# Performance work log

Measured on AMD Instinct MI355X. Metric: run time of the kernel, lower is better.

## Reference

```python
import jax, jax.numpy as jnp
import numpy as np


def setup_inputs() -> dict:
    key = jax.random.key(0)
    ks = jax.random.split(key, 6)
    dim, dt_rank, dim_inner, d_state, channels, batch = 1024, 64, 1024, 128, 64, 8
    rn = lambda k, shape, sc: (jax.random.normal(k, shape, jnp.float32) * sc)
    return {
        "x": rn(ks[0], (batch, channels, dim), 1.0),
        "proj_w": rn(ks[1], (dim, dim), dim ** -0.5),
        "proj_b": jnp.zeros((dim,), jnp.float32),
        "conv_w": rn(ks[2], (channels, channels, 3), (channels * 3) ** -0.5),
        "conv_b": jnp.zeros((channels,), jnp.float32),
        "deltaBC_w": rn(ks[3], (dt_rank + 2 * d_state, dim), dim ** -0.5),
        "dt_proj_w": rn(ks[4], (dim_inner, dt_rank), dt_rank ** -0.5),
        "dt_proj_b": jnp.zeros((dim_inner,), jnp.float32),
        "A_log": jnp.log(jnp.broadcast_to(
            jnp.arange(1, d_state + 1, dtype=jnp.float32), (dim_inner, d_state))),
        "D": jnp.ones((dim_inner,), jnp.float32),
    }


def _silu(x):
    return x * jax.nn.sigmoid(x)


def _selective_scan(x, delta, A, B, C, D):
    # x, delta: (b, l, ed); A: (ed, n); B, C: (b, l, n); D: (ed)
    deltaA = jnp.exp(delta[..., None] * A)                      # (b, l, ed, n)
    BX = delta[..., None] * B[:, :, None, :] * x[..., None]     # (b, l, ed, n)

    def binop(e1, e2):
        a1, b1 = e1
        a2, b2 = e2
        return a1 * a2, a2 * b1 + b2

    # h_t = deltaA_t * h_{t-1} + BX_t  (parallel scan over sequence axis)
    _, hs = jax.lax.associative_scan(binop, (deltaA, BX), axis=1)
    y = jnp.einsum("blen,bln->ble", hs, C) + D * x
    return y


def reference(x, proj_w, proj_b, conv_w, conv_b, deltaBC_w,
              dt_proj_w, dt_proj_b, A_log, D):
    dt_rank = dt_proj_w.shape[1]
    d_state = A_log.shape[1]

    skip = x
    # same self.proj applied to both branches
    x1 = x @ proj_w.T + proj_b
    x2 = x1

    # Conv1d over the feature axis, treating seq positions as channels (L == channels)
    x1 = jax.lax.conv_general_dilated(
        x1, conv_w, window_strides=(1,), padding=[(1, 1)],
        dimension_numbers=("NCH", "OIH", "NCH")) + conv_b[None, :, None]
    x1 = _silu(x1)

    # SSM
    A = -jnp.exp(A_log)
    dbc = x1 @ deltaBC_w.T                                      # (b, l, dt_rank + 2n)
    delta = dbc[..., :dt_rank]
    Bm = dbc[..., dt_rank:dt_rank + d_state]
    Cm = dbc[..., dt_rank + d_state:]
    delta = jax.nn.softplus(delta @ dt_proj_w.T + dt_proj_b)    # (b, l, ed)
    y = _selective_scan(x1, delta, A, Bm, Cm, D)

    out = y * _silu(x2) + skip
    return out @ proj_w.T + proj_b
```

## Files before the change

### kernel.cpp

```cpp
#include <hip/hip_runtime.h>
#include <hip/hip_bf16.h>
#include <math.h>

typedef __hip_bfloat16 bf16;
typedef __attribute__((ext_vector_type(8))) short bf16x8;
typedef __attribute__((ext_vector_type(4))) float f32x4;

#define DIM     1024
#define DT_RANK 64
#define D_STATE 128
#define CHAN    64
#define BATCH   8
#define ROWS    (BATCH*CHAN)
#define DBC_N   (DT_RANK + 2*D_STATE)

#define SZ_X    (ROWS*DIM)
#define SZ_PW   (DIM*DIM)
#define SZ_PB   (DIM)
#define SZ_CW   (CHAN*CHAN*3)
#define SZ_CB   (CHAN)
#define SZ_DBCW (DBC_N*DIM)
#define SZ_DTW  (DIM*DT_RANK)
#define SZ_DTB  (DIM)
#define SZ_ALOG (DIM*D_STATE)
#define SZ_D    (DIM)

#define O0 0
#define O1 (O0+SZ_X)
#define O2 (O1+SZ_PW)
#define O3 (O2+SZ_PB)
#define O4 (O3+SZ_CW)
#define O5 (O4+SZ_CB)
#define O6 (O5+SZ_DBCW)
#define O7 (O6+SZ_DTW)
#define O8 (O7+SZ_DTB)
#define O9 (O8+SZ_ALOG)
#define TOTAL (O9+SZ_D)

__device__ __forceinline__ unsigned short f2b(float v) {
    bf16 t = __float2bfloat16(v);
    return *reinterpret_cast<unsigned short*>(&t);
}
__device__ __forceinline__ float b162f(unsigned short s) {
    return __uint_as_float(((unsigned)s) << 16);
}

__global__ __launch_bounds__(256) void convert_kernel(
    const void* __restrict__ s0, const void* __restrict__ s1,
    const void* __restrict__ s2, const void* __restrict__ s3,
    const void* __restrict__ s4, const void* __restrict__ s5,
    const void* __restrict__ s6, const void* __restrict__ s7,
    const void* __restrict__ s8, const void* __restrict__ s9,
    float* __restrict__ dstf, bf16* __restrict__ dstb,
    int* __restrict__ flag, const unsigned* __restrict__ dsrc)
{
    const int isb = (dsrc[0] == 0x3F803F80u) ? 1 : 0;
    if (blockIdx.x == 0 && threadIdx.x == 0) *flag = isb;
    int idx = (blockIdx.x * 256 + threadIdx.x) * 4;
    if (idx >= TOTAL) return;
    const void* src; int base;
    if      (idx < O1) { src = s0; base = O0; }
    else if (idx < O2) { src = s1; base = O1; }
    else if (idx < O3) { src = s2; base = O2; }
    else if (idx < O4) { src = s3; base = O3; }
    else if (idx < O5) { src = s4; base = O4; }
    else if (idx < O6) { src = s5; base = O5; }
    else if (idx < O7) { src = s6; base = O6; }
    else if (idx < O8) { src = s7; base = O7; }
    else if (idx < O9) { src = s8; base = O8; }
    else               { src = s9; base = O9; }
    const int rel = idx - base;
    float4 v;
    if (isb) {
        ushort4 s = *reinterpret_cast<const ushort4*>((const bf16*)src + rel);
        v.x = b162f(s.x); v.y = b162f(s.y); v.z = b162f(s.z); v.w = b162f(s.w);
    } else {
        v = *reinterpret_cast<const float4*>((const float*)src + rel);
    }
    *reinterpret_cast<float4*>(&dstf[idx]) = v;
    ushort4 u; u.x = f2b(v.x); u.y = f2b(v.y); u.z = f2b(v.z); u.w = f2b(v.w);
    *reinterpret_cast<ushort4*>(&dstb[idx]) = u;
}

template<int ACT, int OUTMODE, int K>
__global__ __launch_bounds__(256) void gemm_mfma(
    const bf16* __restrict__ A, const bf16* __restrict__ B,
    const float* __restrict__ bias, void* __restrict__ C0, bf16* __restrict__ C1,
    int lda, int ldb, int ldc, const int* __restrict__ flagp)
{
    __shared__ float red[4][32][36];
    const int l  = threadIdx.x & 63;
    const int w  = threadIdx.x >> 6;
    const int m0 = blockIdx.y * 32;
    const int n0 = blockIdx.x * 32;
    const int fr = l & 15;
    const int ko = (l >> 4) * 8;

    const bf16* Abase = A + (size_t)(m0 + fr) * lda + ko;
    const bf16* Bbase = B + (size_t)(n0 + fr) * ldb + ko;

    f32x4 acc00 = {}, acc01 = {}, acc10 = {}, acc11 = {};

    #pragma unroll 4
    for (int ks = w; ks * 32 < K; ks += 4) {
        const int k0 = ks * 32;
        bf16x8 a0 = *reinterpret_cast<const bf16x8*>(Abase + k0);
        bf16x8 a1 = *reinterpret_cast<const bf16x8*>(Abase + (size_t)16 * lda + k0);
        bf16x8 b0 = *reinterpret_cast<const bf16x8*>(Bbase + k0);
        bf16x8 b1 = *reinterpret_cast<const bf16x8*>(Bbase + (size_t)16 * ldb + k0);
        acc00 = __builtin_amdgcn_mfma_f32_16x16x32_bf16(a0, b0, acc00, 0, 0, 0);
        acc01 = __builtin_amdgcn_mfma_f32_16x16x32_bf16(a0, b1, acc01, 0, 0, 0);
        acc10 = __builtin_amdgcn_mfma_f32_16x16x32_bf16(a1, b0, acc10, 0, 0, 0);
        acc11 = __builtin_amdgcn_mfma_f32_16x16x32_bf16(a1, b1, acc11, 0, 0, 0);
    }

    {
        const int cr = (l >> 4) * 4;
        const int cc = l & 15;
        #pragma unroll
        for (int v = 0; v < 4; ++v) {
            red[w][cr + v][cc]           = acc00[v];
            red[w][cr + v][16 + cc]      = acc01[v];
            red[w][16 + cr + v][cc]      = acc10[v];
            red[w][16 + cr + v][16 + cc] = acc11[v];
        }
    }
    __syncthreads();

    const int t = threadIdx.x;
    const int r = t >> 3;
    const int c = (t & 7) * 4;
    float o[4];
    #pragma unroll
    for (int q = 0; q < 4; ++q) {
        float s = red[0][r][c + q] + red[1][r][c + q]
                + red[2][r][c + q] + red[3][r][c + q];
        if (bias) s += bias[n0 + c + q];
        if (ACT == 1) s = (s > 20.0f) ? s : log1pf(__expf(s));
        o[q] = s;
    }
    const int m = m0 + r, nn = n0 + c;
    const size_t off = (size_t)m * ldc + nn;
    if (OUTMODE == 0) {
        *reinterpret_cast<float4*>((float*)C0 + off) = make_float4(o[0], o[1], o[2], o[3]);
    } else if (OUTMODE == 2) {
        *reinterpret_cast<float4*>((float*)C0 + off) = make_float4(o[0], o[1], o[2], o[3]);
        ushort4 u; u.x = f2b(o[0]); u.y = f2b(o[1]); u.z = f2b(o[2]); u.w = f2b(o[3]);
        *reinterpret_cast<ushort4*>(C1 + off) = u;
    } else {
        if (*flagp) {
            ushort4 u; u.x = f2b(o[0]); u.y = f2b(o[1]); u.z = f2b(o[2]); u.w = f2b(o[3]);
            *reinterpret_cast<ushort4*>((bf16*)C0 + off) = u;
        } else {
            *reinterpret_cast<float4*>((float*)C0 + off) = make_float4(o[0], o[1], o[2], o[3]);
        }
    }
}

__global__ __launch_bounds__(256) void conv_silu_kernel(
    const float* __restrict__ xin, const float* __restrict__ cw,
    const float* __restrict__ cb, float* __restrict__ xout,
    bf16* __restrict__ xout_bf)
{
    const int o   = blockIdx.x;
    const int n   = blockIdx.y;
    const int tid = threadIdx.x;
    const int h0  = tid * 4;
    const float* xrow = xin + (size_t)n * CHAN * DIM;
    const float* wrow = cw + o * CHAN * 3;
    float acc0 = 0.f, acc1 = 0.f, acc2 = 0.f, acc3 = 0.f;
    #pragma unroll 4
    for (int i = 0; i < CHAN; ++i) {
        const float* xr = xrow + (size_t)i * DIM;
        const float4 xv = *reinterpret_cast<const float4*>(&xr[h0]);
        const float left  = (h0 > 0)        ? xr[h0 - 1] : 0.0f;
        const float right = (h0 + 4 < DIM)  ? xr[h0 + 4] : 0.0f;
        const float w0 = wrow[i * 3 + 0];
        const float w1 = wrow[i * 3 + 1];
        const float w2 = wrow[i * 3 + 2];
        acc0 = fmaf(left, w0, fmaf(xv.x, w1, fmaf(xv.y, w2, acc0)));
        acc1 = fmaf(xv.x, w0, fmaf(xv.y, w1, fmaf(xv.z, w2, acc1)));
        acc2 = fmaf(xv.y, w0, fmaf(xv.z, w1, fmaf(xv.w, w2, acc2)));
        acc3 = fmaf(xv.z, w0, fmaf(xv.w, w1, fmaf(right, w2, acc3)));
    }
    const float bb = cb[o];
    size_t base = (size_t)(n * CHAN + o) * DIM + h0;
    float v0 = acc0 + bb, v1 = acc1 + bb, v2 = acc2 + bb, v3 = acc3 + bb;
    v0 = v0 / (1.0f + __expf(-v0));
    v1 = v1 / (1.0f + __expf(-v1));
    v2 = v2 / (1.0f + __expf(-v2));
    v3 = v3 / (1.0f + __expf(-v3));
    *reinterpret_cast<float4*>(&xout[base]) = make_float4(v0, v1, v2, v3);
    ushort4 u; u.x = f2b(v0); u.y = f2b(v1); u.z = f2b(v2); u.w = f2b(v3);
    *reinterpret_cast<ushort4*>(&xout_bf[base]) = u;
}

__device__ __forceinline__ float sum8_dpp(float x) {
    int v;
    v = __builtin_amdgcn_update_dpp(0, __float_as_int(x), 0x111, 0xf, 0xf, true);
    x += __int_as_float(v);
    v = __builtin_amdgcn_update_dpp(0, __float_as_int(x), 0x112, 0xf, 0xf, true);
    x += __int_as_float(v);
    v = __builtin_amdgcn_update_dpp(0, __float_as_int(x), 0x114, 0xf, 0xf, true);
    x += __int_as_float(v);
    return x;
}

#define EPW 2
__global__ __launch_bounds__(256) void scan_kernel(
    const float* __restrict__ xskip,
    const float* __restrict__ x2,
    const float* __restrict__ xc,
    const float* __restrict__ dbc,
    const float* __restrict__ delta,
    const float* __restrict__ A_log,
    const float* __restrict__ Dp,
    bf16*        __restrict__ outp)
{
    __shared__ float sDB[4][CHAN][4];
    __shared__ float sPart[4][EPW][CHAN][8];
    const int w    = threadIdx.x >> 6;
    const int lane = threadIdx.x & 63;
    const int bb   = blockIdx.x >> 7;
    const int eb   = (blockIdx.x & 127) * (4 * EPW) + w * EPW;
    const int r0   = bb * CHAN;
    const int r    = r0 + lane;

    const float2 dlt2 = *reinterpret_cast<const float2*>(&delta[(size_t)r * DIM + eb]);
    const float2 xv2  = *reinterpret_cast<const float2*>(&xc   [(size_t)r * DIM + eb]);
    const float2 x22  = *reinterpret_cast<const float2*>(&x2   [(size_t)r * DIM + eb]);
    const float2 xs2  = *reinterpret_cast<const float2*>(&xskip[(size_t)r * DIM + eb]);
    const float2 dv2  = *reinterpret_cast<const float2*>(&Dp[eb]);

    const float C_LOG2E = 1.44269504f;
    const float2 alA = *reinterpret_cast<const float2*>(&A_log[(size_t)(eb    ) * D_STATE + 2 * lane]);
    const float2 alB = *reinterpret_cast<const float2*>(&A_log[(size_t)(eb + 1) * D_STATE + 2 * lane]);
    const float a00 = -__expf(alA.x) * C_LOG2E;
    const float a01 = -__expf(alA.y) * C_LOG2E;
    const float a10 = -__expf(alB.x) * C_LOG2E;
    const float a11 = -__expf(alB.y) * C_LOG2E;
    const float ga0 = x22.x / (1.0f + __expf(-x22.x));
    const float ga1 = x22.y / (1.0f + __expf(-x22.y));
    const float fb0 = fmaf(dv2.x * xv2.x, ga0, xs2.x);
    const float fb1 = fmaf(dv2.y * xv2.y, ga1, xs2.y);

    *reinterpret_cast<float4*>(&sDB[w][lane][0]) =
        make_float4(dlt2.x, dlt2.x * xv2.x, dlt2.y, dlt2.y * xv2.y);
    __syncthreads();

    float h00 = 0.f, h01 = 0.f, h10 = 0.f, h11 = 0.f;
    const float* bp = dbc + (size_t)r0 * DBC_N + DT_RANK + 2 * lane;
    const float* cp = bp + D_STATE;
    float2 bv = *reinterpret_cast<const float2*>(bp);
    float2 cv = *reinterpret_cast<const float2*>(cp);

    #pragma unroll 4
    for (int l = 0; l < CHAN; ++l) {
        const float* bpn = bp + ((l < CHAN - 1) ? DBC_N : 0);
        const float* cpn = cp + ((l < CHAN - 1) ? DBC_N : 0);
        const float2 bn = *reinterpret_cast<const float2*>(bpn);
        const float2 cn = *reinterpret_cast<const float2*>(cpn);

        const float4 d = *reinterpret_cast<const float4*>(&sDB[w][l][0]);

        const float e00 = exp2f(d.x * a00);
        const float e01 = exp2f(d.x * a01);
        h00 = fmaf(e00, h00, d.y * bv.x);
        h01 = fmaf(e01, h01, d.y * bv.y);
        const float p0 = sum8_dpp(fmaf(h00, cv.x, h01 * cv.y));

        const float e10 = exp2f(d.z * a10);
        const float e11 = exp2f(d.z * a11);
        h10 = fmaf(e10, h10, d.w * bv.x);
        h11 = fmaf(e11, h11, d.w * bv.y);
        const float p1 = sum8_dpp(fmaf(h10, cv.x, h11 * cv.y));

        if ((lane & 7) == 7) {
            const int q = lane >> 3;
            sPart[w][0][l][q] = p0;
            sPart[w][1][l][q] = p1;
        }
        bp = bpn; cp = cpn; bv = bn; cv = cn;
    }
    __syncthreads();

    const float4 q0 = *reinterpret_cast<const float4*>(&sPart[w][0][lane][0]);
    const float4 q1 = *reinterpret_cast<const float4*>(&sPart[w][0][lane][4]);
    const float4 q2 = *reinterpret_cast<const float4*>(&sPart[w][1][lane][0]);
    const float4 q3 = *reinterpret_cast<const float4*>(&sPart[w][1][lane][4]);
    const float y0 = ((q0.x + q0.y) + (q0.z + q0.w)) + ((q1.x + q1.y) + (q1.z + q1.w));
    const float y1 = ((q2.x + q2.y) + (q2.z + q2.w)) + ((q3.x + q3.y) + (q3.z + q3.w));
    ushort2 u;
    u.x = f2b(fmaf(y0, ga0, fb0));
    u.y = f2b(fmaf(y1, ga1, fb1));
    *reinterpret_cast<ushort2*>(&outp[(size_t)r * DIM + eb]) = u;
}

extern "C" void kernel_launch(void* const* d_in, const int* in_sizes, int n_in,
                              void* d_out, int out_size, void* d_ws, size_t ws_size,
                              hipStream_t stream) {
    float* ws   = (float*)d_ws;
    int*   flag = (int*)d_ws;
    float* inF  = ws + 16;
    bf16*  inB  = (bf16*)(inF + TOTAL);

    float* x1_pre = (float*)(inB + TOTAL);
    float* x1c    = x1_pre + (size_t)ROWS * DIM;
    bf16*  x1c_bf = (bf16*)(x1c + (size_t)ROWS * DIM);
    float* dbc    = (float*)(x1c_bf + (size_t)ROWS * DIM);
    bf16*  dbc_bf = (bf16*)(dbc + (size_t)ROWS * DBC_N);
    float* delta  = (float*)(dbc_bf + (size_t)ROWS * DBC_N);
    bf16*  outp_bf= (bf16*)(delta + (size_t)ROWS * DIM);

    convert_kernel<<<(TOTAL / 4 + 255) / 256, 256, 0, stream>>>(
        d_in[0], d_in[1], d_in[2], d_in[3], d_in[4],
        d_in[5], d_in[6], d_in[7], d_in[8], d_in[9],
        inF, inB, flag, (const unsigned*)d_in[9]);

    gemm_mfma<0, 0, DIM><<<dim3(DIM / 32, ROWS / 32), 256, 0, stream>>>(
        inB + O0, inB + O1, inF + O2, x1_pre, nullptr, DIM, DIM, DIM, nullptr);
    conv_silu_kernel<<<dim3(CHAN, BATCH), 256, 0, stream>>>(x1_pre, inF + O3, inF + O4, x1c, x1c_bf);
    gemm_mfma<0, 2, DIM><<<dim3(DBC_N / 32, ROWS / 32), 256, 0, stream>>>(
        x1c_bf, inB + O5, nullptr, dbc, dbc_bf, DIM, DIM, DBC_N, nullptr);
    gemm_mfma<1, 0, DT_RANK><<<dim3(DIM / 32, ROWS / 32), 256, 0, stream>>>(
        dbc_bf, inB + O6, inF + O7, delta, nullptr, DBC_N, DT_RANK, DIM, nullptr);
    scan_kernel<<<dim3(BATCH * (DIM / (4 * EPW))), 256, 0, stream>>>(
        inF + O0, x1_pre, x1c, dbc, delta, inF + O8, inF + O9, outp_bf);
    gemm_mfma<0, 1, DIM><<<dim3(DIM / 32, ROWS / 32), 256, 0, stream>>>(
        outp_bf, inB + O1, inF + O2, d_out, nullptr, DIM, DIM, DIM, flag);
}
```

Before: 96.52 us.

## Stage bf16 B/C in LDS for scan, drop fp32 dbc and x copies

The scan kernel now loads the B/C columns of dbc as bf16 into shared memory once per block and reads them from LDS. Each lane now owns states lane and lane+64 instead of a contiguous pair, so the per-step reduction becomes a full 64-lane DPP sum with a single lane writing y, replacing the 8-way partials. The fp32 dbc output of the deltaBC GEMM, the fp32 copies of x and proj_w from the convert kernel, and the fp32 skip read are all dropped. This cuts global traffic and writes, but B/C and the skip term are now consumed at bf16 precision, and the longer DPP chain adds latency on each scan step.

```diff
diff --git a/kernel.cpp b/kernel.cpp
--- a/kernel.cpp
+++ b/kernel.cpp
@@ -77,7 +77,8 @@
     } else {
         v = *reinterpret_cast<const float4*>((const float*)src + rel);
     }
-    *reinterpret_cast<float4*>(&dstf[idx]) = v;
+    if (idx >= O2)
+        *reinterpret_cast<float4*>(&dstf[idx]) = v;
     ushort4 u; u.x = f2b(v.x); u.y = f2b(v.y); u.z = f2b(v.z); u.w = f2b(v.w);
     *reinterpret_cast<ushort4*>(&dstb[idx]) = u;
 }
@@ -145,6 +146,9 @@
         *reinterpret_cast<float4*>((float*)C0 + off) = make_float4(o[0], o[1], o[2], o[3]);
     } else if (OUTMODE == 2) {
         *reinterpret_cast<float4*>((float*)C0 + off) = make_float4(o[0], o[1], o[2], o[3]);
+        ushort4 u; u.x = f2b(o[0]); u.y = f2b(o[1]); u.z = f2b(o[2]); u.w = f2b(o[3]);
+        *reinterpret_cast<ushort4*>(C1 + off) = u;
+    } else if (OUTMODE == 3) {
         ushort4 u; u.x = f2b(o[0]); u.y = f2b(o[1]); u.z = f2b(o[2]); u.w = f2b(o[3]);
         *reinterpret_cast<ushort4*>(C1 + off) = u;
     } else {
@@ -195,104 +199,106 @@
     *reinterpret_cast<ushort4*>(&xout_bf[base]) = u;
 }
 
-__device__ __forceinline__ float sum8_dpp(float x) {
+__device__ __forceinline__ float sum64_dpp(float x) {
     int v;
-    v = __builtin_amdgcn_update_dpp(0, __float_as_int(x), 0x111, 0xf, 0xf, true);
-    x += __int_as_float(v);
-    v = __builtin_amdgcn_update_dpp(0, __float_as_int(x), 0x112, 0xf, 0xf, true);
-    x += __int_as_float(v);
-    v = __builtin_amdgcn_update_dpp(0, __float_as_int(x), 0x114, 0xf, 0xf, true);
-    x += __int_as_float(v);
+    v = __builtin_amdgcn_update_dpp(0, __float_as_int(x), 0x111, 0xf, 0xf, true); x += __int_as_float(v);
+    v = __builtin_amdgcn_update_dpp(0, __float_as_int(x), 0x112, 0xf, 0xf, true); x += __int_as_float(v);
+    v = __builtin_amdgcn_update_dpp(0, __float_as_int(x), 0x114, 0xf, 0xf, true); x += __int_as_float(v);
+    v = __builtin_amdgcn_update_dpp(0, __float_as_int(x), 0x118, 0xf, 0xf, true); x += __int_as_float(v);
+    v = __builtin_amdgcn_update_dpp(0, __float_as_int(x), 0x142, 0xa, 0xf, true); x += __int_as_float(v);
+    v = __builtin_amdgcn_update_dpp(0, __float_as_int(x), 0x143, 0xc, 0xf, true); x += __int_as_float(v);
     return x;
 }
 
 #define EPW 2
+#define SBPAD 264
 __global__ __launch_bounds__(256) void scan_kernel(
-    const float* __restrict__ xskip,
+    const bf16*  __restrict__ xskip_bf,
     const float* __restrict__ x2,
     const float* __restrict__ xc,
-    const float* __restrict__ dbc,
+    const bf16*  __restrict__ dbc_bf,
     const float* __restrict__ delta,
     const float* __restrict__ A_log,
     const float* __restrict__ Dp,
     bf16*        __restrict__ outp)
 {
+    __shared__ unsigned short sBC[CHAN][SBPAD];
     __shared__ float sDB[4][CHAN][4];
-    __shared__ float sPart[4][EPW][CHAN][8];
+    __shared__ float sY[4][CHAN][2];
     const int w    = threadIdx.x >> 6;
     const int lane = threadIdx.x & 63;
     const int bb   = blockIdx.x >> 7;
-    const int eb   = (blockIdx.x & 127) * (4 * EPW) + w * EPW;
+    const int eb   = (blockIdx.x & 127) * 8 + w * 2;
     const int r0   = bb * CHAN;
     const int r    = r0 + lane;
 
-    const float2 dlt2 = *reinterpret_cast<const float2*>(&delta[(size_t)r * DIM + eb]);
-    const float2 xv2  = *reinterpret_cast<const float2*>(&xc   [(size_t)r * DIM + eb]);
-    const float2 x22  = *reinterpret_cast<const float2*>(&x2   [(size_t)r * DIM + eb]);
-    const float2 xs2  = *reinterpret_cast<const float2*>(&xskip[(size_t)r * DIM + eb]);
-    const float2 dv2  = *reinterpret_cast<const float2*>(&Dp[eb]);
+    {
+        const int row = threadIdx.x >> 2, q = threadIdx.x & 3;
+        const uint4* src = reinterpret_cast<const uint4*>(
+            dbc_bf + (size_t)(r0 + row) * DBC_N + DT_RANK + q * 64);
+        uint4* dst = reinterpret_cast<uint4*>(&sBC[row][q * 64]);
+        #pragma unroll
+        for (int k = 0; k < 8; ++k) dst[k] = src[k];
+    }
+
+    const float2  dlt2 = *reinterpret_cast<const float2*>(&delta[(size_t)r * DIM + eb]);
+    const float2  xv2  = *reinterpret_cast<const float2*>(&xc   [(size_t)r * DIM + eb]);
+    const float2  x22  = *reinterpret_cast<const float2*>(&x2   [(size_t)r * DIM + eb]);
+    const ushort2 xsu  = *reinterpret_cast<const ushort2*>(&xskip_bf[(size_t)r * DIM + eb]);
+    const float2  dv2  = *reinterpret_cast<const float2*>(&Dp[eb]);
 
     const float C_LOG2E = 1.44269504f;
-    const float2 alA = *reinterpret_cast<const float2*>(&A_log[(size_t)(eb    ) * D_STATE + 2 * lane]);
-    const float2 alB = *reinterpret_cast<const float2*>(&A_log[(size_t)(eb + 1) * D_STATE + 2 * lane]);
-    const float a00 = -__expf(alA.x) * C_LOG2E;
-    const float a01 = -__expf(alA.y) * C_LOG2E;
-    const float a10 = -__expf(alB.x) * C_LOG2E;
-    const float a11 = -__expf(alB.y) * C_LOG2E;
+    const float a00 = -__expf(A_log[(size_t)(eb    ) * D_STATE + lane])      * C_LOG2E;
+    const float a01 = -__expf(A_log[(size_t)(eb    ) * D_STATE + 64 + lane]) * C_LOG2E;
+    const float a10 = -__expf(A_log[(size_t)(eb + 1) * D_STATE + lane])      * C_LOG2E;
+    const float a11 = -__expf(A_log[(size_t)(eb + 1) * D_STATE + 64 + lane]) * C_LOG2E;
     const float ga0 = x22.x / (1.0f + __expf(-x22.x));
     const float ga1 = x22.y / (1.0f + __expf(-x22.y));
-    const float fb0 = fmaf(dv2.x * xv2.x, ga0, xs2.x);
-    const float fb1 = fmaf(dv2.y * xv2.y, ga1, xs2.y);
+    const float fb0 = fmaf(dv2.x * xv2.x, ga0, b162f(xsu.x));
+    const float fb1 = fmaf(dv2.y * xv2.y, ga1, b162f(xsu.y));
 
     *reinterpret_cast<float4*>(&sDB[w][lane][0]) =
         make_float4(dlt2.x, dlt2.x * xv2.x, dlt2.y, dlt2.y * xv2.y);
     __syncthreads();
 
     float h00 = 0.f, h01 = 0.f, h10 = 0.f, h11 = 0.f;
-    const float* bp = dbc + (size_t)r0 * DBC_N + DT_RANK + 2 * lane;
-    const float* cp = bp + D_STATE;
-    float2 bv = *reinterpret_cast<const float2*>(bp);
-    float2 cv = *reinterpret_cast<const float2*>(cp);
+    float4 d = *reinterpret_cast<const float4*>(&sDB[w][0][0]);
+    unsigned short b0u = sBC[0][lane],       b1u = sBC[0][64 + lane];
+    unsigned short c0u = sBC[0][128 + lane], c1u = sBC[0][192 + lane];
 
     #pragma unroll 4
     for (int l = 0; l < CHAN; ++l) {
-        const float* bpn = bp + ((l < CHAN - 1) ? DBC_N : 0);
-        const float* cpn = cp + ((l < CHAN - 1) ? DBC_N : 0);
-        const float2 bn = *reinterpret_cast<const float2*>(bpn);
-        const float2 cn = *reinterpret_cast<const float2*>(cpn);
-
-        const float4 d = *reinterpret_cast<const float4*>(&sDB[w][l][0]);
+        const int ln = (l + 1) & 63;
+        const float4 dn = *reinterpret_cast<const float4*>(&sDB[w][ln][0]);
+        const unsigned short b0n = sBC[ln][lane],       b1n = sBC[ln][64 + lane];
+        const unsigned short c0n = sBC[ln][128 + lane], c1n = sBC[ln][192 + lane];
+
+        const float bv0 = b162f(b0u), bv1 = b162f(b1u);
+        const float cv0 = b162f(c0u), cv1 = b162f(c1u);
 
         const float e00 = exp2f(d.x * a00);
         const float e01 = exp2f(d.x * a01);
-        h00 = fmaf(e00, h00, d.y * bv.x);
-        h01 = fmaf(e01, h01, d.y * bv.y);
-        const float p0 = sum8_dpp(fmaf(h00, cv.x, h01 * cv.y));
+        h00 = fmaf(e00, h00, d.y * bv0);
+        h01 = fmaf(e01, h01, d.y * bv1);
+        const float p0 = sum64_dpp(fmaf(h00, cv0, h01 * cv1));
 
         const float e10 = exp2f(d.z * a10);
         const float e11 = exp2f(d.z * a11);
-        h10 = fmaf(e10, h10, d.w * bv.x);
-        h11 = fmaf(e11, h11, d.w * bv.y);
-        const float p1 = sum8_dpp(fmaf(h10, cv.x, h11 * cv.y));
-
-        if ((lane & 7) == 7) {
-            const int q = lane >> 3;
-            sPart[w][0][l][q] = p0;
-            sPart[w][1][l][q] = p1;
-        }
-        bp = bpn; cp = cpn; bv = bn; cv = cn;
+        h10 = fmaf(e10, h10, d.w * bv0);
+        h11 = fmaf(e11, h11, d.w * bv1);
+        const float p1 = sum64_dpp(fmaf(h10, cv0, h11 * cv1));
+
+        if (lane == 63)
+            *reinterpret_cast<float2*>(&sY[w][l][0]) = make_float2(p0, p1);
+
+        d = dn; b0u = b0n; b1u = b1n; c0u = c0n; c1u = c1n;
     }
     __syncthreads();
 
-    const float4 q0 = *reinterpret_cast<const float4*>(&sPart[w][0][lane][0]);
-    const float4 q1 = *reinterpret_cast<const float4*>(&sPart[w][0][lane][4]);
-    const float4 q2 = *reinterpret_cast<const float4*>(&sPart[w][1][lane][0]);
-    const float4 q3 = *reinterpret_cast<const float4*>(&sPart[w][1][lane][4]);
-    const float y0 = ((q0.x + q0.y) + (q0.z + q0.w)) + ((q1.x + q1.y) + (q1.z + q1.w));
-    const float y1 = ((q2.x + q2.y) + (q2.z + q2.w)) + ((q3.x + q3.y) + (q3.z + q3.w));
+    const float2 y = *reinterpret_cast<const float2*>(&sY[w][lane][0]);
     ushort2 u;
-    u.x = f2b(fmaf(y0, ga0, fb0));
-    u.y = f2b(fmaf(y1, ga1, fb1));
+    u.x = f2b(fmaf(y.x, ga0, fb0));
+    u.y = f2b(fmaf(y.y, ga1, fb1));
     *reinterpret_cast<ushort2*>(&outp[(size_t)r * DIM + eb]) = u;
 }
 
@@ -320,12 +326,12 @@
     gemm_mfma<0, 0, DIM><<<dim3(DIM / 32, ROWS / 32), 256, 0, stream>>>(
         inB + O0, inB + O1, inF + O2, x1_pre, nullptr, DIM, DIM, DIM, nullptr);
     conv_silu_kernel<<<dim3(CHAN, BATCH), 256, 0, stream>>>(x1_pre, inF + O3, inF + O4, x1c, x1c_bf);
-    gemm_mfma<0, 2, DIM><<<dim3(DBC_N / 32, ROWS / 32), 256, 0, stream>>>(
-        x1c_bf, inB + O5, nullptr, dbc, dbc_bf, DIM, DIM, DBC_N, nullptr);
+    gemm_mfma<0, 3, DIM><<<dim3(DBC_N / 32, ROWS / 32), 256, 0, stream>>>(
+        x1c_bf, inB + O5, nullptr, nullptr, dbc_bf, DIM, DIM, DBC_N, nullptr);
     gemm_mfma<1, 0, DT_RANK><<<dim3(DIM / 32, ROWS / 32), 256, 0, stream>>>(
         dbc_bf, inB + O6, inF + O7, delta, nullptr, DBC_N, DT_RANK, DIM, nullptr);
     scan_kernel<<<dim3(BATCH * (DIM / (4 * EPW))), 256, 0, stream>>>(
-        inF + O0, x1_pre, x1c, dbc, delta, inF + O8, inF + O9, outp_bf);
+        inB + O0, x1_pre, x1c, dbc_bf, delta, inF + O8, inF + O9, outp_bf);
     gemm_mfma<0, 1, DIM><<<dim3(DIM / 32, ROWS / 32), 256, 0, stream>>>(
         outp_bf, inB + O1, inF + O2, d_out, nullptr, DIM, DIM, DIM, flag);
 }
```

Result: slower. 99.50 us (+3.1%).
